# Performance work log

Hardware: AMD Instinct MI355X
Metric: run time of the kernel (lower is better)

Reference implementation:

```python
import jax, jax.numpy as jnp
import numpy as np

C = 512
C8 = C // 8  # query/key projection dim


def _conv1x1(x, W, b):
    # x: [B,C,H,W], W: [O,C], b: [O] -> [B,O,H,W]
    return jnp.einsum('bchw,oc->bohw', x, W) + b[None, :, None, None]


def setup_inputs() -> dict:
    key = jax.random.key(0)
    ks = jax.random.split(key, 13)
    B, H, Wd = 4, 64, 64
    s = 0.02
    return {
        'x_rgb': jax.random.normal(ks[0], (B, C, H, Wd), jnp.float32),
        'x_dep': jax.random.normal(ks[1], (B, C, H, Wd), jnp.float32),
        'Wq': jax.random.normal(ks[2], (C8, C), jnp.float32) * s,
        'bq': jnp.zeros((C8,), jnp.float32),
        'Wk': jax.random.normal(ks[3], (C8, C), jnp.float32) * s,
        'bk': jnp.zeros((C8,), jnp.float32),
        'Wdq': jax.random.normal(ks[4], (C8, C), jnp.float32) * s,
        'bdq': jnp.zeros((C8,), jnp.float32),
        'Wdk': jax.random.normal(ks[5], (C8, C), jnp.float32) * s,
        'bdk': jnp.zeros((C8,), jnp.float32),
        'Wv': jax.random.normal(ks[6], (C, C), jnp.float32) * s,
        'bv': jnp.zeros((C,), jnp.float32),
        'gamma': jnp.zeros((1,), jnp.float32),
    }


def reference(x_rgb, x_dep, Wq, bq, Wk, bk, Wdq, bdq, Wdk, bdk, Wv, bv, gamma):
    B, Cc, H, Wd = x_rgb.shape
    N = H * Wd
    # 1x1 conv projections, flattened over spatial positions -> [B, c, N]
    q = _conv1x1(x_rgb, Wq, bq).reshape(B, C8, N)
    k = _conv1x1(x_rgb, Wk, bk).reshape(B, C8, N)
    qd = _conv1x1(x_dep, Wdq, bdq).reshape(B, C8, N)
    kd = _conv1x1(x_dep, Wdk, bdk).reshape(B, C8, N)
    # fused dual-stream energy: [B, N, N]
    energy = jnp.einsum('bci,bcj->bij', q, k) + jnp.einsum('bci,bcj->bij', qd, kd)
    attention = jax.nn.softmax(energy, axis=-1)
    v = _conv1x1(x_rgb, Wv, bv).reshape(B, Cc, N)
    # out[b,c,i] = sum_j v[b,c,j] * attention[b,i,j]
    out = jnp.einsum('bcj,bij->bci', v, attention).reshape(B, Cc, H, Wd)
    return gamma[0] * out + x_rgb
```

## Files before the change

kernel.cpp:

```cpp
#include <hip/hip_runtime.h>
#include <math.h>

#define B_ 4
#define C_ 512
#define D_ 128
#define N_ 4096

typedef short s4v __attribute__((ext_vector_type(4)));
typedef short s8v __attribute__((ext_vector_type(8)));
typedef float f4v __attribute__((ext_vector_type(4)));

__device__ __forceinline__ unsigned short f2bf(float x) {
    union { float f; unsigned u; } v; v.f = x;
    unsigned r = v.u + 0x7FFF + ((v.u >> 16) & 1);
    return (unsigned short)(r >> 16);
}
__device__ __forceinline__ float bf2f(unsigned short h) {
    union { unsigned u; float f; } v; v.u = ((unsigned)h) << 16; return v.f;
}

__global__ __launch_bounds__(256) void cvt_w_kernel(
    const float* __restrict__ Wq,  const float* __restrict__ bq,
    const float* __restrict__ Wk,  const float* __restrict__ bk,
    const float* __restrict__ Wdq, const float* __restrict__ bdq,
    const float* __restrict__ Wdk, const float* __restrict__ bdk,
    const float* __restrict__ Wv,  const float* __restrict__ bv,
    unsigned short* __restrict__ Wb, float* __restrict__ biasb)
{
    int t = blockIdx.x * 256 + threadIdx.x;
    int e0 = t * 8;
    int row = e0 >> 9, c = e0 & 511;
    const float* src; int r0;
    if (row < 64)       { src = Wq;  r0 = row; }
    else if (row < 128) { src = Wk;  r0 = row - 64; }
    else if (row < 640) { src = Wv;  r0 = row - 128; }
    else if (row < 704) { src = Wdq; r0 = row - 640; }
    else                { src = Wdk; r0 = row - 704; }
    const float* p = src + (size_t)r0 * 512 + c;
    s8v o;
    #pragma unroll
    for (int u = 0; u < 8; ++u) ((unsigned short*)&o)[u] = f2bf(p[u]);
    *(s8v*)&Wb[e0] = o;
    if (blockIdx.x == 0) {
        #pragma unroll
        for (int s = 0; s < 3; ++s) {
            int o2 = threadIdx.x + 256 * s;
            float v;
            if (o2 < 64)       v = bq[o2];
            else if (o2 < 128) v = bk[o2 - 64];
            else if (o2 < 640) v = bv[o2 - 128];
            else if (o2 < 704) v = bdq[o2 - 640];
            else               v = bdk[o2 - 704];
            biasb[o2] = v;
        }
    }
}

__global__ __launch_bounds__(256) void gemm_kernel(
    const unsigned short* __restrict__ Wb, const float* __restrict__ biasb,
    const float* __restrict__ x_rgb, const float* __restrict__ x_dep,
    unsigned short* __restrict__ Q, unsigned short* __restrict__ K,
    unsigned short* __restrict__ V)
{
    __shared__ __align__(16) unsigned short Ws[128 * 64];
    __shared__ __align__(16) unsigned short Xs[128 * 72];
    const int b  = blockIdx.x >> 5;
    const int i0 = (blockIdx.x & 31) * 128;
    const int by = blockIdx.y;
    const int mbase = by * 128;
    const int st = (by == 5);
    const int t = threadIdx.x, w = t >> 6;
    const int lane = t & 63, col = lane & 15, quad = lane >> 4;
    const int mh = (w & 1) * 64, nh = (w >> 1) * 64;
    const int c4x = t >> 4, i4x = t & 15;

    const unsigned short* Wg = Wb + (size_t)mbase * 512;
    const float* Xsrc = (st ? x_dep : x_rgb) + (size_t)b * C_ * N_;

    f4v acc[4][4];
    #pragma unroll
    for (int mt = 0; mt < 4; ++mt)
        #pragma unroll
        for (int nt = 0; nt < 4; ++nt) acc[mt][nt] = (f4v){0.f, 0.f, 0.f, 0.f};

    for (int kc = 0; kc < 8; ++kc) {
        const int k0 = kc * 64;
        s8v wt[4];
        float4 xr[2][4];
        #pragma unroll
        for (int s = 0; s < 4; ++s) {
            int lin = t + 256 * s;
            int row = lin >> 3, g = lin & 7;
            wt[s] = *(const s8v*)&Wg[(size_t)row * 512 + k0 + g * 8];
        }
        #pragma unroll
        for (int ih2 = 0; ih2 < 2; ++ih2) {
            const float* xp = Xsrc + (size_t)(k0 + c4x * 4) * N_
                            + i0 + ih2 * 64 + i4x * 4;
            xr[ih2][0] = *(const float4*)(xp);
            xr[ih2][1] = *(const float4*)(xp + N_);
            xr[ih2][2] = *(const float4*)(xp + 2 * N_);
            xr[ih2][3] = *(const float4*)(xp + 3 * N_);
        }
        __syncthreads();
        #pragma unroll
        for (int s = 0; s < 4; ++s) {
            int lin = t + 256 * s;
            int row = lin >> 3, g = lin & 7;
            int soff = row * 64 + ((g ^ (row & 7)) * 8);
            *(s8v*)&Ws[soff] = wt[s];
        }
        #pragma unroll
        for (int ih2 = 0; ih2 < 2; ++ih2) {
            #pragma unroll
            for (int j = 0; j < 4; ++j) {
                s4v pj = { (short)f2bf(xr[ih2][0][j]), (short)f2bf(xr[ih2][1][j]),
                           (short)f2bf(xr[ih2][2][j]), (short)f2bf(xr[ih2][3][j]) };
                *(s4v*)&Xs[(ih2 * 64 + i4x * 4 + j) * 72 + c4x * 4] = pj;
            }
        }
        __syncthreads();
        #pragma unroll
        for (int kk = 0; kk < 2; ++kk) {
            const int gq = kk * 4 + quad;
            s8v af[4], bf[4];
            #pragma unroll
            for (int mt = 0; mt < 4; ++mt) {
                int r = mh + mt * 16 + col;
                af[mt] = *(const s8v*)&Ws[r * 64 + ((gq ^ (r & 7)) * 8)];
            }
            #pragma unroll
            for (int nt = 0; nt < 4; ++nt) {
                int r = nh + nt * 16 + col;
                bf[nt] = *(const s8v*)&Xs[r * 72 + gq * 8];
            }
            #pragma unroll
            for (int nt = 0; nt < 4; ++nt)
                #pragma unroll
                for (int mt = 0; mt < 4; ++mt)
                    acc[mt][nt] = __builtin_amdgcn_mfma_f32_16x16x32_bf16(
                        af[mt], bf[nt], acc[mt][nt], 0, 0, 0);
        }
    }

    const int mlo0 = mbase + mh;
    #pragma unroll
    for (int mt = 0; mt < 4; ++mt) {
        const int mlo = mlo0 + mt * 16;
        f4v bi = *(const f4v*)&biasb[mlo + quad * 4];
        if (mlo < 128 || mlo >= 640) {
            unsigned short* dst; int dbase;
            if (mlo < 64)       { dst = Q; dbase = mlo; }
            else if (mlo < 128) { dst = K; dbase = mlo - 64; }
            else if (mlo < 704) { dst = Q; dbase = 64 + (mlo - 640); }
            else                { dst = K; dbase = 64 + (mlo - 704); }
            #pragma unroll
            for (int nt = 0; nt < 4; ++nt) {
                int i = i0 + nh + nt * 16 + col;
                s4v pk = { (short)f2bf(acc[mt][nt][0] + bi[0]),
                           (short)f2bf(acc[mt][nt][1] + bi[1]),
                           (short)f2bf(acc[mt][nt][2] + bi[2]),
                           (short)f2bf(acc[mt][nt][3] + bi[3]) };
                *(s4v*)&dst[((size_t)b * N_ + i) * D_ + dbase + quad * 4] = pk;
            }
        } else {
            int c0 = mlo - 128 + quad * 4;
            #pragma unroll
            for (int nt = 0; nt < 4; ++nt) {
                int i = i0 + nh + nt * 16 + col;
                #pragma unroll
                for (int r = 0; r < 4; ++r)
                    V[((size_t)b * C_ + c0 + r) * N_ + i] =
                        f2bf(acc[mt][nt][r] + bi[r]);
            }
        }
    }
}

__global__ __launch_bounds__(256, 2) void attn_kernel(
    const unsigned short* __restrict__ Q, const unsigned short* __restrict__ K,
    const unsigned short* __restrict__ V,
    unsigned short* __restrict__ O_ws, float* __restrict__ l_ws)
{
    __shared__ __align__(16) unsigned short Ks[32 * 136];
    __shared__ __align__(16) unsigned short Ps[64 * 40];
    __shared__ __align__(16) unsigned short Vs[512 * 32];
    __shared__ float lred[2][64];

    const int id  = blockIdx.x;
    const int grp = id & 7;
    const int b   = grp & 3;
    const int jh  = grp >> 2;
    const int it  = id >> 3;
    const int i0  = it * 64;
    const int jb  = jh * 2048;
    const int t = threadIdx.x, w = t >> 6;
    const int lane = t & 63, col = lane & 15, quad = lane >> 4;
    const int ih = w & 1, jq = w >> 1;

    const unsigned short* Kg = K + (size_t)b * N_ * D_;
    const unsigned short* Vg = V + (size_t)b * C_ * N_;

    s8v qf[2][4];
    #pragma unroll
    for (int ig = 0; ig < 2; ++ig) {
        const unsigned short* qr =
            Q + ((size_t)b * N_ + i0 + ih * 32 + ig * 16 + col) * D_ + quad * 8;
        #pragma unroll
        for (int kk = 0; kk < 4; ++kk) qf[ig][kk] = *(const s8v*)(qr + kk * 32);
    }

    f4v accO[4][8];
    #pragma unroll
    for (int rt = 0; rt < 4; ++rt)
        #pragma unroll
        for (int ct = 0; ct < 8; ++ct) accO[rt][ct] = (f4v){0.f, 0.f, 0.f, 0.f};
    float lsum[2] = {0.f, 0.f};

    for (int tt = 0; tt < 64; ++tt) {
        const int j0 = jb + tt * 32;
        s8v kt[2], vt[8];
        #pragma unroll
        for (int s = 0; s < 2; ++s) {
            int gi = t + 256 * s;
            kt[s] = *(const s8v*)&Kg[(size_t)(j0 + (gi >> 4)) * D_ + (gi & 15) * 8];
        }
        #pragma unroll
        for (int s = 0; s < 8; ++s) {
            int gi = t + 256 * s;
            vt[s] = *(const s8v*)&Vg[(size_t)(gi >> 2) * N_ + j0 + (gi & 3) * 8];
        }
        asm volatile("s_waitcnt lgkmcnt(0)" ::: "memory");
        __builtin_amdgcn_s_barrier();
        #pragma unroll
        for (int s = 0; s < 2; ++s) {
            int gi = t + 256 * s;
            *(s8v*)&Ks[(gi >> 4) * 136 + (gi & 15) * 8] = kt[s];
        }
        asm volatile("s_waitcnt lgkmcnt(0)" ::: "memory");
        __builtin_amdgcn_s_barrier();
        f4v s0 = (f4v){0.f, 0.f, 0.f, 0.f};
        f4v s1 = (f4v){0.f, 0.f, 0.f, 0.f};
        #pragma unroll
        for (int kk = 0; kk < 4; ++kk) {
            s8v kf = *(const s8v*)&Ks[(jq * 16 + col) * 136 + kk * 32 + quad * 8];
            s0 = __builtin_amdgcn_mfma_f32_16x16x32_bf16(kf, qf[0][kk], s0, 0, 0, 0);
            s1 = __builtin_amdgcn_mfma_f32_16x16x32_bf16(kf, qf[1][kk], s1, 0, 0, 0);
        }
        #pragma unroll
        for (int ig = 0; ig < 2; ++ig) {
            f4v sv = ig ? s1 : s0;
            s4v p; float ls = 0.f;
            #pragma unroll
            for (int r = 0; r < 4; ++r) {
                float e = __expf(sv[r]);
                ls += e;
                p[r] = (short)f2bf(e);
            }
            lsum[ig] += ls;
            *(s4v*)&Ps[(ih * 32 + ig * 16 + col) * 40 + jq * 16 + quad * 4] = p;
        }
        #pragma unroll
        for (int s = 0; s < 8; ++s) {
            int gi = t + 256 * s;
            int c = gi >> 2, g = gi & 3;
            int sw = (g + c + (c >> 2)) & 3;
            *(s8v*)&Vs[c * 32 + sw * 8] = vt[s];
        }
        asm volatile("s_waitcnt lgkmcnt(0)" ::: "memory");
        __builtin_amdgcn_s_barrier();
        s8v pf[4];
        #pragma unroll
        for (int rt = 0; rt < 4; ++rt)
            pf[rt] = *(const s8v*)&Ps[(rt * 16 + col) * 40 + quad * 8];
        __builtin_amdgcn_s_setprio(1);
        #pragma unroll
        for (int ct = 0; ct < 8; ++ct) {
            int row = w * 128 + ct * 16 + col;
            int sw = (quad + row + (row >> 2)) & 3;
            s8v vf = *(const s8v*)&Vs[row * 32 + sw * 8];
            #pragma unroll
            for (int rt = 0; rt < 4; ++rt)
                accO[rt][ct] = __builtin_amdgcn_mfma_f32_16x16x32_bf16(pf[rt], vf, accO[rt][ct], 0, 0, 0);
        }
        __builtin_amdgcn_s_setprio(0);
    }

    #pragma unroll
    for (int ig = 0; ig < 2; ++ig) {
        float v = lsum[ig];
        v += __shfl_xor(v, 16);
        v += __shfl_xor(v, 32);
        if (quad == 0) lred[jq][ih * 32 + ig * 16 + col] = v;
    }
    __syncthreads();
    if (t < 64)
        l_ws[((size_t)jh * B_ + b) * N_ + i0 + t] = lred[0][t] + lred[1][t];

    const size_t wbase =
        ((((size_t)jh * B_ + b) * 64 + it) * 4 + w) * 8192;
    #pragma unroll
    for (int ct = 0; ct < 8; ++ct)
        #pragma unroll
        for (int rt = 0; rt < 4; ++rt) {
            s4v pk = { (short)f2bf(accO[rt][ct][0]), (short)f2bf(accO[rt][ct][1]),
                       (short)f2bf(accO[rt][ct][2]), (short)f2bf(accO[rt][ct][3]) };
            *(s4v*)&O_ws[wbase + (size_t)(ct * 4 + rt) * 256 + lane * 4] = pk;
        }
}

__global__ __launch_bounds__(256) void combine_kernel(
    const unsigned short* __restrict__ O_ws, const float* __restrict__ l_ws,
    const float* __restrict__ x_rgb, const float* __restrict__ gamma,
    float* __restrict__ out)
{
    const size_t half = (size_t)B_ * 64 * 4 * 8192;
    const int bx = blockIdx.x;
    const int ct0 = (bx & 3) * 2;
    const int w  = (bx >> 2) & 3;
    const int it = (bx >> 4) & 63;
    const int b  = bx >> 10;
    const int t  = threadIdx.x;
    const int rt = t >> 6, l = t & 63;
    const int c_sub = l >> 2, qd = l & 3;

    const int i = it * 64 + rt * 16 + qd * 4;
    float4 l0 = *(const float4*)&l_ws[(size_t)b * N_ + i];
    float4 l1 = *(const float4*)&l_ws[(size_t)(B_ + b) * N_ + i];
    float4 linv = { 1.f / (l0.x + l1.x), 1.f / (l0.y + l1.y),
                    1.f / (l0.z + l1.z), 1.f / (l0.w + l1.w) };
    float g = gamma[0];

    #pragma unroll
    for (int u = 0; u < 2; ++u) {
        const int ct = ct0 + u;
        const int c = w * 128 + ct * 16 + c_sub;
        const size_t seg = (((size_t)b * 64 + it) * 4 + w) * 8192
                         + (size_t)(ct * 4 + rt) * 256 + (qd * 16 + c_sub) * 4;
        s4v o0 = *(const s4v*)&O_ws[seg];
        s4v o1 = *(const s4v*)&O_ws[half + seg];
        size_t base = ((size_t)b * C_ + c) * N_ + i;
        float4 x4 = *(const float4*)&x_rgb[base];
        float4 r;
        r.x = g * (bf2f((unsigned short)o0[0]) + bf2f((unsigned short)o1[0])) * linv.x + x4.x;
        r.y = g * (bf2f((unsigned short)o0[1]) + bf2f((unsigned short)o1[1])) * linv.y + x4.y;
        r.z = g * (bf2f((unsigned short)o0[2]) + bf2f((unsigned short)o1[2])) * linv.z + x4.z;
        r.w = g * (bf2f((unsigned short)o0[3]) + bf2f((unsigned short)o1[3])) * linv.w + x4.w;
        *(float4*)&out[base] = r;
    }
}

extern "C" void kernel_launch(void* const* d_in, const int* in_sizes, int n_in,
                              void* d_out, int out_size, void* d_ws, size_t ws_size,
                              hipStream_t stream) {
    (void)in_sizes; (void)n_in; (void)out_size; (void)ws_size;
    const float* x_rgb = (const float*)d_in[0];
    const float* x_dep = (const float*)d_in[1];
    const float* Wq    = (const float*)d_in[2];
    const float* bq    = (const float*)d_in[3];
    const float* Wk    = (const float*)d_in[4];
    const float* bk    = (const float*)d_in[5];
    const float* Wdq   = (const float*)d_in[6];
    const float* bdq   = (const float*)d_in[7];
    const float* Wdk   = (const float*)d_in[8];
    const float* bdk   = (const float*)d_in[9];
    const float* Wv    = (const float*)d_in[10];
    const float* bv    = (const float*)d_in[11];
    const float* gamma = (const float*)d_in[12];
    float* out = (float*)d_out;

    unsigned short* Q     = (unsigned short*)d_ws;
    unsigned short* K     = Q + (size_t)B_ * N_ * D_;
    unsigned short* V     = K + (size_t)B_ * N_ * D_;
    unsigned short* Wb    = V + (size_t)B_ * C_ * N_;
    float*          biasb = (float*)(Wb + 768 * 512);
    unsigned short* XtO   = (unsigned short*)(biasb + 1024);
    float*          l_ws  = (float*)(XtO + (size_t)2 * B_ * C_ * N_);

    cvt_w_kernel<<<dim3(192), 256, 0, stream>>>(
        Wq, bq, Wk, bk, Wdq, bdq, Wdk, bdk, Wv, bv, Wb, biasb);
    gemm_kernel<<<dim3(128, 6), 256, 0, stream>>>(Wb, biasb, x_rgb, x_dep, Q, K, V);
    attn_kernel<<<dim3(512), 256, 0, stream>>>(Q, K, V, XtO, l_ws);
    combine_kernel<<<dim3(4096), 256, 0, stream>>>(XtO, l_ws, x_rgb, gamma, out);
}
```

Measured before the change: 272.8 us.

## Fuse split-K combine into attention kernel via atomic ticket per tile

Removes the separate combine kernel. Each attention block writes its partial output and row sums, then takes an atomic ticket on a per-tile counter. The second of the two split-j blocks to finish reads its partner's partial, normalizes, adds the residual and writes the output. This saves a kernel launch and one read of this block's own partial from workspace. In exchange it adds a memset, threadfences and a partially serialized tail in the last-finishing blocks.

```diff
diff --git a/kernel.cpp b/kernel.cpp
--- a/kernel.cpp
+++ b/kernel.cpp
@@ -180,12 +180,16 @@
 __global__ __launch_bounds__(256, 2) void attn_kernel(
     const unsigned short* __restrict__ Q, const unsigned short* __restrict__ K,
     const unsigned short* __restrict__ V,
-    unsigned short* __restrict__ O_ws, float* __restrict__ l_ws)
+    unsigned short* __restrict__ O_ws, float* __restrict__ l_ws,
+    const float* __restrict__ x_rgb, const float* __restrict__ gamma,
+    float* __restrict__ out, unsigned int* __restrict__ cnt)
 {
     __shared__ __align__(16) unsigned short Ks[32 * 136];
     __shared__ __align__(16) unsigned short Ps[64 * 40];
     __shared__ __align__(16) unsigned short Vs[512 * 32];
     __shared__ float lred[2][64];
+    __shared__ float lredT[64];
+    __shared__ int ticket_s;
 
     const int id  = blockIdx.x;
     const int grp = id & 7;
@@ -294,8 +298,11 @@
         if (quad == 0) lred[jq][ih * 32 + ig * 16 + col] = v;
     }
     __syncthreads();
-    if (t < 64)
-        l_ws[((size_t)jh * B_ + b) * N_ + i0 + t] = lred[0][t] + lred[1][t];
+    if (t < 64) {
+        float lv = lred[0][t] + lred[1][t];
+        l_ws[((size_t)jh * B_ + b) * N_ + i0 + t] = lv;
+        lredT[t] = lv;
+    }
 
     const size_t wbase =
         ((((size_t)jh * B_ + b) * 64 + it) * 4 + w) * 8192;
@@ -307,46 +314,38 @@
                        (short)f2bf(accO[rt][ct][2]), (short)f2bf(accO[rt][ct][3]) };
             *(s4v*)&O_ws[wbase + (size_t)(ct * 4 + rt) * 256 + lane * 4] = pk;
         }
-}
-
-__global__ __launch_bounds__(256) void combine_kernel(
-    const unsigned short* __restrict__ O_ws, const float* __restrict__ l_ws,
-    const float* __restrict__ x_rgb, const float* __restrict__ gamma,
-    float* __restrict__ out)
-{
-    const size_t half = (size_t)B_ * 64 * 4 * 8192;
-    const int bx = blockIdx.x;
-    const int ct0 = (bx & 3) * 2;
-    const int w  = (bx >> 2) & 3;
-    const int it = (bx >> 4) & 63;
-    const int b  = bx >> 10;
-    const int t  = threadIdx.x;
-    const int rt = t >> 6, l = t & 63;
-    const int c_sub = l >> 2, qd = l & 3;
-
-    const int i = it * 64 + rt * 16 + qd * 4;
-    float4 l0 = *(const float4*)&l_ws[(size_t)b * N_ + i];
-    float4 l1 = *(const float4*)&l_ws[(size_t)(B_ + b) * N_ + i];
-    float4 linv = { 1.f / (l0.x + l1.x), 1.f / (l0.y + l1.y),
-                    1.f / (l0.z + l1.z), 1.f / (l0.w + l1.w) };
-    float g = gamma[0];
-
-    #pragma unroll
-    for (int u = 0; u < 2; ++u) {
-        const int ct = ct0 + u;
-        const int c = w * 128 + ct * 16 + c_sub;
-        const size_t seg = (((size_t)b * 64 + it) * 4 + w) * 8192
-                         + (size_t)(ct * 4 + rt) * 256 + (qd * 16 + c_sub) * 4;
-        s4v o0 = *(const s4v*)&O_ws[seg];
-        s4v o1 = *(const s4v*)&O_ws[half + seg];
-        size_t base = ((size_t)b * C_ + c) * N_ + i;
-        float4 x4 = *(const float4*)&x_rgb[base];
-        float4 r;
-        r.x = g * (bf2f((unsigned short)o0[0]) + bf2f((unsigned short)o1[0])) * linv.x + x4.x;
-        r.y = g * (bf2f((unsigned short)o0[1]) + bf2f((unsigned short)o1[1])) * linv.y + x4.y;
-        r.z = g * (bf2f((unsigned short)o0[2]) + bf2f((unsigned short)o1[2])) * linv.z + x4.z;
-        r.w = g * (bf2f((unsigned short)o0[3]) + bf2f((unsigned short)o1[3])) * linv.w + x4.w;
-        *(float4*)&out[base] = r;
+
+    __threadfence();
+    __syncthreads();
+    if (t == 0) ticket_s = (int)atomicAdd(&cnt[b * 64 + it], 1u);
+    __syncthreads();
+    if (ticket_s == 0) return;
+    __threadfence();
+
+    const int jho = 1 - jh;
+    const size_t pbase =
+        ((((size_t)jho * B_ + b) * 64 + it) * 4 + w) * 8192;
+    const float* lop = &l_ws[((size_t)jho * B_ + b) * N_ + i0];
+    const float g = gamma[0];
+    #pragma unroll
+    for (int ct = 0; ct < 8; ++ct) {
+        const int c = w * 128 + ct * 16 + col;
+        #pragma unroll
+        for (int rt = 0; rt < 4; ++rt) {
+            const int il = rt * 16 + quad * 4;
+            s4v po = *(const s4v*)&O_ws[pbase + (size_t)(ct * 4 + rt) * 256 + lane * 4];
+            float4 lo = *(const float4*)(lop + il);
+            float lw0 = lredT[il], lw1 = lredT[il + 1],
+                  lw2 = lredT[il + 2], lw3 = lredT[il + 3];
+            size_t base = ((size_t)b * C_ + c) * N_ + i0 + il;
+            float4 x4 = *(const float4*)&x_rgb[base];
+            float4 r;
+            r.x = g * (accO[rt][ct][0] + bf2f((unsigned short)po[0])) / (lw0 + lo.x) + x4.x;
+            r.y = g * (accO[rt][ct][1] + bf2f((unsigned short)po[1])) / (lw1 + lo.y) + x4.y;
+            r.z = g * (accO[rt][ct][2] + bf2f((unsigned short)po[2])) / (lw2 + lo.z) + x4.z;
+            r.w = g * (accO[rt][ct][3] + bf2f((unsigned short)po[3])) / (lw3 + lo.w) + x4.w;
+            *(float4*)&out[base] = r;
+        }
     }
 }
 
@@ -374,12 +373,14 @@
     unsigned short* V     = K + (size_t)B_ * N_ * D_;
     unsigned short* Wb    = V + (size_t)B_ * C_ * N_;
     float*          biasb = (float*)(Wb + 768 * 512);
-    unsigned short* XtO   = (unsigned short*)(biasb + 1024);
-    float*          l_ws  = (float*)(XtO + (size_t)2 * B_ * C_ * N_);
-
+    unsigned short* O_ws  = (unsigned short*)(biasb + 1024);
+    float*          l_ws  = (float*)(O_ws + (size_t)2 * B_ * C_ * N_);
+    unsigned int*   cnt   = (unsigned int*)(l_ws + (size_t)2 * B_ * N_);
+
+    hipMemsetAsync(cnt, 0, 256 * sizeof(unsigned int), stream);
     cvt_w_kernel<<<dim3(192), 256, 0, stream>>>(
         Wq, bq, Wk, bk, Wdq, bdq, Wdk, bdk, Wv, bv, Wb, biasb);
     gemm_kernel<<<dim3(128, 6), 256, 0, stream>>>(Wb, biasb, x_rgb, x_dep, Q, K, V);
-    attn_kernel<<<dim3(512), 256, 0, stream>>>(Q, K, V, XtO, l_ws);
-    combine_kernel<<<dim3(4096), 256, 0, stream>>>(XtO, l_ws, x_rgb, gamma, out);
-}
+    attn_kernel<<<dim3(512), 256, 0, stream>>>(Q, K, V, O_ws, l_ws,
+                                               x_rgb, gamma, out, cnt);
+}
```

Result: slower. 380.0 us (+39.3%).

## Fuse combine into attention by dropping split-KV and using 32-row query tiles

Applied to the files above, without the earlier changes.

The attention kernel no longer splits the key range in two halves. Each block now handles 32 query rows over all 4096 keys, so it can normalize by the full row sum and write gamma*O/l + x_rgb directly. The output is transposed through shared memory (reusing the V tile buffer) for coalesced stores. This removes the bf16 partial-output workspace round trip and the separate combine launch. In exchange, each K/V tile loaded into shared memory now feeds only 32 query rows instead of 64, halving reuse of the K and V streams.

```diff
diff --git a/kernel.cpp b/kernel.cpp
--- a/kernel.cpp
+++ b/kernel.cpp
@@ -180,20 +180,20 @@
 __global__ __launch_bounds__(256, 2) void attn_kernel(
     const unsigned short* __restrict__ Q, const unsigned short* __restrict__ K,
     const unsigned short* __restrict__ V,
-    unsigned short* __restrict__ O_ws, float* __restrict__ l_ws)
+    const float* __restrict__ x_rgb, const float* __restrict__ gamma,
+    float* __restrict__ out)
 {
     __shared__ __align__(16) unsigned short Ks[32 * 136];
-    __shared__ __align__(16) unsigned short Ps[64 * 40];
+    __shared__ __align__(16) unsigned short Ps[32 * 40];
     __shared__ __align__(16) unsigned short Vs[512 * 32];
-    __shared__ float lred[2][64];
+    __shared__ float lred[2][32];
 
     const int id  = blockIdx.x;
     const int grp = id & 7;
     const int b   = grp & 3;
-    const int jh  = grp >> 2;
-    const int it  = id >> 3;
-    const int i0  = it * 64;
-    const int jb  = jh * 2048;
+    const int itl = grp >> 2;
+    const int it  = (id >> 3) * 2 + itl;
+    const int i0  = it * 32;
     const int t = threadIdx.x, w = t >> 6;
     const int lane = t & 63, col = lane & 15, quad = lane >> 4;
     const int ih = w & 1, jq = w >> 1;
@@ -201,24 +201,23 @@
     const unsigned short* Kg = K + (size_t)b * N_ * D_;
     const unsigned short* Vg = V + (size_t)b * C_ * N_;
 
-    s8v qf[2][4];
-    #pragma unroll
-    for (int ig = 0; ig < 2; ++ig) {
+    s8v qf[4];
+    {
         const unsigned short* qr =
-            Q + ((size_t)b * N_ + i0 + ih * 32 + ig * 16 + col) * D_ + quad * 8;
-        #pragma unroll
-        for (int kk = 0; kk < 4; ++kk) qf[ig][kk] = *(const s8v*)(qr + kk * 32);
-    }
-
-    f4v accO[4][8];
-    #pragma unroll
-    for (int rt = 0; rt < 4; ++rt)
+            Q + ((size_t)b * N_ + i0 + ih * 16 + col) * D_ + quad * 8;
+        #pragma unroll
+        for (int kk = 0; kk < 4; ++kk) qf[kk] = *(const s8v*)(qr + kk * 32);
+    }
+
+    f4v accO[2][8];
+    #pragma unroll
+    for (int rt = 0; rt < 2; ++rt)
         #pragma unroll
         for (int ct = 0; ct < 8; ++ct) accO[rt][ct] = (f4v){0.f, 0.f, 0.f, 0.f};
-    float lsum[2] = {0.f, 0.f};
-
-    for (int tt = 0; tt < 64; ++tt) {
-        const int j0 = jb + tt * 32;
+    float lsum = 0.f;
+
+    for (int tt = 0; tt < 128; ++tt) {
+        const int j0 = tt * 32;
         s8v kt[2], vt[8];
         #pragma unroll
         for (int s = 0; s < 2; ++s) {
@@ -240,25 +239,21 @@
         asm volatile("s_waitcnt lgkmcnt(0)" ::: "memory");
         __builtin_amdgcn_s_barrier();
         f4v s0 = (f4v){0.f, 0.f, 0.f, 0.f};
-        f4v s1 = (f4v){0.f, 0.f, 0.f, 0.f};
         #pragma unroll
         for (int kk = 0; kk < 4; ++kk) {
             s8v kf = *(const s8v*)&Ks[(jq * 16 + col) * 136 + kk * 32 + quad * 8];
-            s0 = __builtin_amdgcn_mfma_f32_16x16x32_bf16(kf, qf[0][kk], s0, 0, 0, 0);
-            s1 = __builtin_amdgcn_mfma_f32_16x16x32_bf16(kf, qf[1][kk], s1, 0, 0, 0);
-        }
-        #pragma unroll
-        for (int ig = 0; ig < 2; ++ig) {
-            f4v sv = ig ? s1 : s0;
+            s0 = __builtin_amdgcn_mfma_f32_16x16x32_bf16(kf, qf[kk], s0, 0, 0, 0);
+        }
+        {
             s4v p; float ls = 0.f;
             #pragma unroll
             for (int r = 0; r < 4; ++r) {
-                float e = __expf(sv[r]);
+                float e = __expf(s0[r]);
                 ls += e;
                 p[r] = (short)f2bf(e);
             }
-            lsum[ig] += ls;
-            *(s4v*)&Ps[(ih * 32 + ig * 16 + col) * 40 + jq * 16 + quad * 4] = p;
+            lsum += ls;
+            *(s4v*)&Ps[(ih * 16 + col) * 40 + jq * 16 + quad * 4] = p;
         }
         #pragma unroll
         for (int s = 0; s < 8; ++s) {
@@ -269,9 +264,9 @@
         }
         asm volatile("s_waitcnt lgkmcnt(0)" ::: "memory");
         __builtin_amdgcn_s_barrier();
-        s8v pf[4];
-        #pragma unroll
-        for (int rt = 0; rt < 4; ++rt)
+        s8v pf[2];
+        #pragma unroll
+        for (int rt = 0; rt < 2; ++rt)
             pf[rt] = *(const s8v*)&Ps[(rt * 16 + col) * 40 + quad * 8];
         __builtin_amdgcn_s_setprio(1);
         #pragma unroll
@@ -280,73 +275,61 @@
             int sw = (quad + row + (row >> 2)) & 3;
             s8v vf = *(const s8v*)&Vs[row * 32 + sw * 8];
             #pragma unroll
-            for (int rt = 0; rt < 4; ++rt)
+            for (int rt = 0; rt < 2; ++rt)
                 accO[rt][ct] = __builtin_amdgcn_mfma_f32_16x16x32_bf16(pf[rt], vf, accO[rt][ct], 0, 0, 0);
         }
         __builtin_amdgcn_s_setprio(0);
     }
 
-    #pragma unroll
-    for (int ig = 0; ig < 2; ++ig) {
-        float v = lsum[ig];
+    {
+        float v = lsum;
         v += __shfl_xor(v, 16);
         v += __shfl_xor(v, 32);
-        if (quad == 0) lred[jq][ih * 32 + ig * 16 + col] = v;
+        if (quad == 0) lred[jq][ih * 16 + col] = v;
     }
     __syncthreads();
-    if (t < 64)
-        l_ws[((size_t)jh * B_ + b) * N_ + i0 + t] = lred[0][t] + lred[1][t];
-
-    const size_t wbase =
-        ((((size_t)jh * B_ + b) * 64 + it) * 4 + w) * 8192;
-    #pragma unroll
-    for (int ct = 0; ct < 8; ++ct)
-        #pragma unroll
-        for (int rt = 0; rt < 4; ++rt) {
-            s4v pk = { (short)f2bf(accO[rt][ct][0]), (short)f2bf(accO[rt][ct][1]),
-                       (short)f2bf(accO[rt][ct][2]), (short)f2bf(accO[rt][ct][3]) };
-            *(s4v*)&O_ws[wbase + (size_t)(ct * 4 + rt) * 256 + lane * 4] = pk;
-        }
-}
-
-__global__ __launch_bounds__(256) void combine_kernel(
-    const unsigned short* __restrict__ O_ws, const float* __restrict__ l_ws,
-    const float* __restrict__ x_rgb, const float* __restrict__ gamma,
-    float* __restrict__ out)
-{
-    const size_t half = (size_t)B_ * 64 * 4 * 8192;
-    const int bx = blockIdx.x;
-    const int ct0 = (bx & 3) * 2;
-    const int w  = (bx >> 2) & 3;
-    const int it = (bx >> 4) & 63;
-    const int b  = bx >> 10;
-    const int t  = threadIdx.x;
-    const int rt = t >> 6, l = t & 63;
-    const int c_sub = l >> 2, qd = l & 3;
-
-    const int i = it * 64 + rt * 16 + qd * 4;
-    float4 l0 = *(const float4*)&l_ws[(size_t)b * N_ + i];
-    float4 l1 = *(const float4*)&l_ws[(size_t)(B_ + b) * N_ + i];
-    float4 linv = { 1.f / (l0.x + l1.x), 1.f / (l0.y + l1.y),
-                    1.f / (l0.z + l1.z), 1.f / (l0.w + l1.w) };
-    float g = gamma[0];
-
-    #pragma unroll
-    for (int u = 0; u < 2; ++u) {
-        const int ct = ct0 + u;
-        const int c = w * 128 + ct * 16 + c_sub;
-        const size_t seg = (((size_t)b * 64 + it) * 4 + w) * 8192
-                         + (size_t)(ct * 4 + rt) * 256 + (qd * 16 + c_sub) * 4;
-        s4v o0 = *(const s4v*)&O_ws[seg];
-        s4v o1 = *(const s4v*)&O_ws[half + seg];
-        size_t base = ((size_t)b * C_ + c) * N_ + i;
-        float4 x4 = *(const float4*)&x_rgb[base];
-        float4 r;
-        r.x = g * (bf2f((unsigned short)o0[0]) + bf2f((unsigned short)o1[0])) * linv.x + x4.x;
-        r.y = g * (bf2f((unsigned short)o0[1]) + bf2f((unsigned short)o1[1])) * linv.y + x4.y;
-        r.z = g * (bf2f((unsigned short)o0[2]) + bf2f((unsigned short)o1[2])) * linv.z + x4.z;
-        r.w = g * (bf2f((unsigned short)o0[3]) + bf2f((unsigned short)o1[3])) * linv.w + x4.w;
-        *(float4*)&out[base] = r;
+
+    const float g = gamma[0];
+    float* Tw = (float*)((char*)Vs + w * 4608);
+    float4 lq0 = *(const float4*)&lred[0][quad * 4];
+    float4 lq1 = *(const float4*)&lred[1][quad * 4];
+    float4 lq2 = *(const float4*)&lred[0][16 + quad * 4];
+    float4 lq3 = *(const float4*)&lred[1][16 + quad * 4];
+    float4 linv0 = { 1.f / (lq0.x + lq1.x), 1.f / (lq0.y + lq1.y),
+                     1.f / (lq0.z + lq1.z), 1.f / (lq0.w + lq1.w) };
+    float4 linv1 = { 1.f / (lq2.x + lq3.x), 1.f / (lq2.y + lq3.y),
+                     1.f / (lq2.z + lq3.z), 1.f / (lq2.w + lq3.w) };
+    #pragma unroll
+    for (int cc = 0; cc < 4; ++cc) {
+        #pragma unroll
+        for (int u = 0; u < 2; ++u) {
+            const int ct = cc * 2 + u;
+            const int lc = u * 16 + col;
+            #pragma unroll
+            for (int rt = 0; rt < 2; ++rt) {
+                const float4 li = rt ? linv1 : linv0;
+                const int slot = (rt * 4 + quad) ^ (lc & 7);
+                float4 val = { g * accO[rt][ct][0] * li.x,
+                               g * accO[rt][ct][1] * li.y,
+                               g * accO[rt][ct][2] * li.z,
+                               g * accO[rt][ct][3] * li.w };
+                *(float4*)&Tw[lc * 36 + slot * 4] = val;
+            }
+        }
+        asm volatile("s_waitcnt lgkmcnt(0)" ::: "memory");
+        const int gr = lane & 7, csl = lane >> 3;
+        #pragma unroll
+        for (int p = 0; p < 4; ++p) {
+            const int lc = p * 8 + csl;
+            const int slot = gr ^ (lc & 7);
+            float4 o4 = *(const float4*)&Tw[lc * 36 + slot * 4];
+            const int c = w * 128 + cc * 32 + lc;
+            size_t base = ((size_t)b * C_ + c) * N_ + i0 + gr * 4;
+            float4 x4 = *(const float4*)&x_rgb[base];
+            float4 r4 = { o4.x + x4.x, o4.y + x4.y, o4.z + x4.z, o4.w + x4.w };
+            *(float4*)&out[base] = r4;
+        }
+        asm volatile("s_waitcnt lgkmcnt(0)" ::: "memory");
     }
 }
 
@@ -374,12 +357,9 @@
     unsigned short* V     = K + (size_t)B_ * N_ * D_;
     unsigned short* Wb    = V + (size_t)B_ * C_ * N_;
     float*          biasb = (float*)(Wb + 768 * 512);
-    unsigned short* XtO   = (unsigned short*)(biasb + 1024);
-    float*          l_ws  = (float*)(XtO + (size_t)2 * B_ * C_ * N_);
 
     cvt_w_kernel<<<dim3(192), 256, 0, stream>>>(
         Wq, bq, Wk, bk, Wdq, bdq, Wdk, bdk, Wv, bv, Wb, biasb);
     gemm_kernel<<<dim3(128, 6), 256, 0, stream>>>(Wb, biasb, x_rgb, x_dep, Q, K, V);
-    attn_kernel<<<dim3(512), 256, 0, stream>>>(Q, K, V, XtO, l_ws);
-    combine_kernel<<<dim3(4096), 256, 0, stream>>>(XtO, l_ws, x_rgb, gamma, out);
-}
+    attn_kernel<<<dim3(512), 256, 0, stream>>>(Q, K, V, x_rgb, gamma, out);
+}
```

Result: slower. 314.7 us (+15.4%).
